# Kernel tuning notes

Measured on AMD Instinct MI355X. Metric: run time of the kernel, lower is better.

The kernel has to match this reference:

```python
import jax, jax.numpy as jnp
import numpy as np

T = 8192          # total prefill tokens (single sequence, cu_seqlens=[0,T])
H = 16            # local num heads (k == v heads)
D = 128           # head_k_dim == head_v_dim
K = 4             # causal conv kernel width
CHUNK = 64        # chunk size used by chunk_kda
EPS = 1e-6


def setup_inputs() -> dict:
    key = jax.random.key(0)
    ks = jax.random.split(key, 6)
    return {
        "mixed_qkv": jax.random.normal(ks[0], (T, 3 * H * D), dtype=jnp.float32),
        "forget_gate": jax.random.normal(ks[1], (T, H * D), dtype=jnp.float32),
        "beta": jax.random.normal(ks[2], (T, H), dtype=jnp.float32),
        "conv_weights": jax.random.normal(ks[3], (3 * H * D, K), dtype=jnp.float32) * 0.1,
        "dt_bias": jax.random.normal(ks[4], (H, D), dtype=jnp.float32),
        "alog": jax.random.normal(ks[5], (H,), dtype=jnp.float32),
    }


def _l2norm(x):
    return x * jax.lax.rsqrt(jnp.sum(x * x, axis=-1, keepdims=True) + EPS)


def _causal_conv1d(x, w):
    # x: [T, C], w: [C, K] depthwise causal conv + SiLU (causal_conv1d_fn)
    xpad = jnp.pad(x, ((K - 1, 0), (0, 0)))
    out = sum(xpad[j:j + T] * w[:, j] for j in range(K))
    return jax.nn.silu(out)


def _kda_forward(mixed_qkv, forget_gate, beta, conv_weights, dt_bias, alog):
    x = _causal_conv1d(mixed_qkv, conv_weights)               # [T, 3*H*D]
    q, k, v = jnp.split(x, [H * D, 2 * H * D], axis=-1)
    q = _l2norm(q.reshape(T, H, D)) * (D ** -0.5)             # scale = head_k_dim^-0.5
    k = _l2norm(k.reshape(T, H, D))
    v = v.reshape(T, H, D)
    # fused_kda_gate: g = -exp(A_log) * softplus(g_raw + dt_bias), per (head, dim)
    g = -jnp.exp(alog)[None, :, None] * jax.nn.softplus(
        forget_gate.reshape(T, H, D) + dt_bias[None])
    decay = jnp.exp(g)                                        # [T, H, D]
    b = jax.nn.sigmoid(beta)                                  # [T, H]

    def step(S, inp):
        # S: [H, Dk, Dv]
        q_t, k_t, v_t, d_t, b_t = inp
        S = S * d_t[:, :, None]                               # per-dim forget gate on key dim
        kmem = jnp.einsum('hk,hkv->hv', k_t, S)
        delta = b_t[:, None] * (v_t - kmem)                   # beta-scaled delta rule
        S = S + jnp.einsum('hk,hv->hkv', k_t, delta)
        o_t = jnp.einsum('hk,hkv->hv', q_t, S)
        return S, o_t

    @jax.checkpoint
    def chunk_fn(S, ch):
        return jax.lax.scan(step, S, ch)

    NC = T // CHUNK
    chunked = lambda a: a.reshape(NC, CHUNK, H, D)
    S0 = jnp.zeros((H, D, D), dtype=jnp.float32)
    _, o = jax.lax.scan(chunk_fn, S0,
                        (chunked(q), chunked(k), chunked(v), chunked(decay),
                         b.reshape(NC, CHUNK, H)))
    return o.reshape(T, H, D)


def reference(mixed_qkv, forget_gate, beta, conv_weights, dt_bias, alog):
    return _kda_forward(mixed_qkv, forget_gate, beta, conv_weights, dt_bias, alog)
```

## Files before the change

### kernel.cpp

```cpp
#include <hip/hip_runtime.h>
#include <math.h>

#define NH 16
#define HD 128
#define CH1 2048
#define CH3 6144
#define CK 64
#define NC 128
#define PCH 132
#define MP 68

#define QT_OFF  0u
#define KBT_OFF 16777216u
#define U0_OFF  33554432u
#define Z_OFF   50331648u
#define W_OFF   67108864u
#define ECG_OFF 75497472u
#define SLAB_OFF 75759616u

__global__ __launch_bounds__(1024, 4)
void kda_chunk(const float* __restrict__ mixed, const float* __restrict__ fg,
               const float* __restrict__ beta, const float* __restrict__ cw,
               const float* __restrict__ dtb, const float* __restrict__ alog,
               float* __restrict__ qt_g, float* __restrict__ kbt_g,
               float* __restrict__ u0_g, float* __restrict__ z_g,
               float* __restrict__ w_g, float* __restrict__ ecg_g) {
  __shared__ float lds[36032];
  float* kL  = lds;
  float* qL  = lds + 8448;
  float* cgL = lds + 16896;
  float* ML  = lds + 25344;
  float* NT  = lds + 29696;
  float* GB  = lds + 34048;
  float* bL  = lds + 34816;
  float* nrm = lds + 34880;

  const int tid = threadIdx.x;
  const int bid = blockIdx.x;
  const int c = bid >> 4, h = bid & 15;
  const int t0 = c * CK;
  const float ea = __expf(alog[h]);

  {
    size_t wb = (size_t)bid * 4096;
#pragma unroll
    for (int i = 0; i < 4; ++i) w_g[wb + tid + 1024 * i] = 0.f;
  }

  for (int it = 0; it < 8; ++it) {
    int cell = tid + (it << 10);
    int d = cell & 127, t = cell >> 7;
    float x = fg[(size_t)(t0 + t) * CH1 + h * HD + d] + dtb[h * HD + d];
    float sp = (x > 20.f) ? x : log1pf(__expf(x));
    cgL[t * PCH + d] = -ea * sp;
  }
  if (tid < 64) bL[tid] = 1.f / (1.f + __expf(-beta[(size_t)(t0 + tid) * NH + h]));
  __syncthreads();

  if (tid < 128) {
    float a = 0.f;
    for (int t = 0; t < 64; ++t) { a += cgL[t * PCH + tid]; cgL[t * PCH + tid] = a; }
    ecg_g[(size_t)bid * 128 + tid] = __expf(a);
  }

  for (int it = 0; it < 16; ++it) {
    int cell = tid + (it << 10);
    int d = cell & 127, sec = (cell >> 7) & 1, t = cell >> 8;
    int ch = sec * CH1 + h * HD + d;
    float4 w4 = ((const float4*)cw)[ch];
    int rbase = t0 + t - 3;
    float acc;
    if (rbase >= 0) {
      const float* mp = mixed + (size_t)rbase * CH3 + ch;
      acc = mp[0] * w4.x + mp[CH3] * w4.y + mp[2 * CH3] * w4.z + mp[3 * CH3] * w4.w;
    } else {
      acc = 0.f;
      if (rbase + 0 >= 0) acc += mixed[(size_t)(rbase + 0) * CH3 + ch] * w4.x;
      if (rbase + 1 >= 0) acc += mixed[(size_t)(rbase + 1) * CH3 + ch] * w4.y;
      if (rbase + 2 >= 0) acc += mixed[(size_t)(rbase + 2) * CH3 + ch] * w4.z;
      acc += mixed[(size_t)(rbase + 3) * CH3 + ch] * w4.w;
    }
    acc = acc / (1.f + __expf(-acc));
    float* dst = (sec == 0) ? qL : kL;
    dst[t * PCH + d] = acc;
  }
  __syncthreads();

  {
    int sec = tid >> 9, t = (tid >> 3) & 63, r = tid & 7;
    const float* src = (sec == 0) ? qL : kL;
    float s = 0.f;
#pragma unroll
    for (int i = 0; i < 4; ++i) {
      float4 v = *(const float4*)(src + t * PCH + r * 16 + i * 4);
      s += v.x * v.x + v.y * v.y + v.z * v.z + v.w * v.w;
    }
    nrm[tid] = s;
  }
  __syncthreads();
  if (tid < 128) {
    int sec = tid >> 6, t = tid & 63;
    float s = 0.f;
#pragma unroll
    for (int r = 0; r < 8; ++r) s += nrm[sec * 512 + t * 8 + r];
    float inv = rsqrtf(s + 1e-6f);
    if (sec == 0) inv *= 0.08838834764831845f;
    nrm[1024 + tid] = inv;
  }
  __syncthreads();
  for (int it = 0; it < 4; ++it) {
    int f4 = tid + (it << 10);
    int sec = f4 >> 11, t = (f4 >> 5) & 63, d4 = f4 & 31;
    float* dst = (sec == 0) ? qL : kL;
    float inv = nrm[1024 + sec * 64 + t];
    float4 v = *(float4*)(dst + t * PCH + d4 * 4);
    v.x *= inv; v.y *= inv; v.z *= inv; v.w *= inv;
    *(float4*)(dst + t * PCH + d4 * 4) = v;
  }
  __syncthreads();

  {
    int tW = tid >> 4, g = tid & 15;
    size_t qb = (size_t)bid * 8192 + (size_t)(g >> 1) * 1024 + tW * 16 + (g & 1) * 8;
    size_t kb = (size_t)bid * 8192;
#pragma unroll
    for (int i = 0; i < 2; ++i) {
      int d = g * 8 + 4 * i;
      float4 qv = *(const float4*)(qL + tW * PCH + d);
      float4 cg4 = *(const float4*)(cgL + tW * PCH + d);
      float4 o;
      o.x = qv.x * __expf(cg4.x); o.y = qv.y * __expf(cg4.y);
      o.z = qv.z * __expf(cg4.z); o.w = qv.w * __expf(cg4.w);
      *(float4*)(qt_g + qb + 4 * i) = o;
      float4 kv = *(const float4*)(kL + tW * PCH + d);
      float4 c63 = *(const float4*)(cgL + 63 * PCH + d);
      kbt_g[kb + (size_t)(d + 0) * 64 + tW] = kv.x * __expf(c63.x - cg4.x);
      kbt_g[kb + (size_t)(d + 1) * 64 + tW] = kv.y * __expf(c63.y - cg4.y);
      kbt_g[kb + (size_t)(d + 2) * 64 + tW] = kv.z * __expf(c63.z - cg4.z);
      kbt_g[kb + (size_t)(d + 3) * 64 + tW] = kv.w * __expf(c63.w - cg4.w);
    }
  }

  if (tid < 544) {
    int L = tid >> 2, dh = tid & 3;
    int tt = (int)((sqrtf(8.f * L + 1.f) - 1.f) * 0.5f);
    while ((tt + 1) * (tt + 2) / 2 <= L) ++tt;
    while (tt * (tt + 1) / 2 > L) --tt;
    int ss = L - tt * (tt + 1) / 2;
    int taD = tt * 4, saD = ss * 4;
    float accA[16], accW[16];
#pragma unroll
    for (int i = 0; i < 16; ++i) { accA[i] = 0.f; accW[i] = 0.f; }
    for (int s4 = 0; s4 < 8; ++s4) {
      int d = (dh << 5) + (((s4 + L + (dh << 1)) & 7) << 2);
      float ks4v[4][4], cs4v[4][4];
#pragma unroll
      for (int j = 0; j < 4; ++j) {
        *(float4*)ks4v[j] = *(const float4*)(kL + (saD + j) * PCH + d);
        *(float4*)cs4v[j] = *(const float4*)(cgL + (saD + j) * PCH + d);
      }
#pragma unroll
      for (int i = 0; i < 4; ++i) {
        float kt4[4], qt4[4], ct4[4];
        *(float4*)kt4 = *(const float4*)(kL + (taD + i) * PCH + d);
        *(float4*)qt4 = *(const float4*)(qL + (taD + i) * PCH + d);
        *(float4*)ct4 = *(const float4*)(cgL + (taD + i) * PCH + d);
#pragma unroll
        for (int j = 0; j < 4; ++j)
#pragma unroll
          for (int dd = 0; dd < 4; ++dd) {
            float diff = ct4[dd] - cs4v[j][dd];
            float e = __expf(fminf(diff, 0.f));
            float m = e * ks4v[j][dd];
            accA[i * 4 + j] += kt4[dd] * m;
            accW[i * 4 + j] += qt4[dd] * m;
          }
      }
    }
#pragma unroll
    for (int i = 0; i < 16; ++i) {
      accA[i] += __shfl_xor(accA[i], 1);
      accA[i] += __shfl_xor(accA[i], 2);
      accW[i] += __shfl_xor(accW[i], 1);
      accW[i] += __shfl_xor(accW[i], 2);
    }
    if (dh == 0) {
      size_t wb = (size_t)bid * 4096;
#pragma unroll
      for (int i = 0; i < 4; ++i)
#pragma unroll
        for (int j = 0; j < 4; ++j) {
          int t = taD + i, s = saD + j;
          if (s < t) ML[t * MP + s] = bL[t] * accA[i * 4 + j];
          float wv = (s <= t) ? accW[i * 4 + j] : 0.f;
          w_g[wb + (size_t)(s >> 3) * 512 + t * 8 + (s & 7)] = wv;
        }
    }
  }
  __syncthreads();

  for (int i = tid; i < 4352; i += 1024) NT[i] = 0.f;
  __syncthreads();
  if (tid < 64) {
    int b4 = tid >> 4, j = tid & 15, bo = b4 * 16;
    NT[(bo + j) * MP + bo + j] = 1.f;
    for (int t = j + 1; t < 16; ++t) {
      float s = 0.f;
      for (int sx = j; sx < t; ++sx)
        s += ML[(bo + t) * MP + bo + sx] * NT[(bo + j) * MP + bo + sx];
      NT[(bo + j) * MP + bo + t] = -s;
    }
  }
  __syncthreads();
  for (int lev = 1; lev <= 3; ++lev) {
    int nb = 4 - lev;
    for (int idx = tid; idx < nb * 256; idx += 1024) {
      int J = idx >> 8, I = J + lev;
      int i = (idx >> 4) & 15, j = idx & 15;
      float s = 0.f;
      for (int P = J; P < I; ++P)
#pragma unroll 4
        for (int p = 0; p < 16; ++p)
          s += ML[(16 * I + i) * MP + 16 * P + p] * NT[(16 * J + j) * MP + 16 * P + p];
      GB[J * 256 + i * 16 + j] = s;
    }
    __syncthreads();
    for (int idx = tid; idx < nb * 256; idx += 1024) {
      int J = idx >> 8, I = J + lev;
      int i = (idx >> 4) & 15, j = idx & 15;
      float s = 0.f;
#pragma unroll 4
      for (int p = 0; p < 16; ++p)
        s += NT[(16 * I + p) * MP + 16 * I + i] * GB[J * 256 + p * 16 + j];
      NT[(16 * J + j) * MP + 16 * I + i] = -s;
    }
    __syncthreads();
  }

  {
    int tW = tid >> 4, g = tid & 15;
    float b = bL[tW];
#pragma unroll
    for (int i = 0; i < 2; ++i) {
      int d = g * 8 + 4 * i;
      float4 kv = *(const float4*)(kL + tW * PCH + d);
      float4 cg4 = *(const float4*)(cgL + tW * PCH + d);
      float4 r;
      r.x = b * kv.x * __expf(cg4.x); r.y = b * kv.y * __expf(cg4.y);
      r.z = b * kv.z * __expf(cg4.z); r.w = b * kv.w * __expf(cg4.w);
      *(float4*)(qL + tW * PCH + d) = r;
    }
  }
  __syncthreads();
  {
    int t2 = tid >> 5, c4 = tid & 31;
    float acc[2][4];
#pragma unroll
    for (int i = 0; i < 2; ++i)
#pragma unroll
      for (int j = 0; j < 4; ++j) acc[i][j] = 0.f;
    for (int s = 0; s < 64; ++s) {
      float2 nv = *(const float2*)(NT + s * MP + t2 * 2);
      float rv[4];
      *(float4*)rv = *(const float4*)(qL + s * PCH + c4 * 4);
#pragma unroll
      for (int j = 0; j < 4; ++j) {
        acc[0][j] += nv.x * rv[j];
        acc[1][j] += nv.y * rv[j];
      }
    }
    size_t zb = (size_t)bid * 8192 + (size_t)(c4 >> 2) * 1024 + (c4 & 3) * 4;
#pragma unroll
    for (int i = 0; i < 2; ++i) {
      float4 o; o.x = acc[i][0]; o.y = acc[i][1]; o.z = acc[i][2]; o.w = acc[i][3];
      *(float4*)(z_g + zb + (size_t)(t2 * 2 + i) * 16) = o;
    }
  }
  __syncthreads();

  for (int it = 0; it < 8; ++it) {
    int cell = tid + (it << 10);
    int d = cell & 127, t = cell >> 7;
    int ch = 2 * CH1 + h * HD + d;
    float4 w4 = ((const float4*)cw)[ch];
    int rbase = t0 + t - 3;
    float acc;
    if (rbase >= 0) {
      const float* mp = mixed + (size_t)rbase * CH3 + ch;
      acc = mp[0] * w4.x + mp[CH3] * w4.y + mp[2 * CH3] * w4.z + mp[3 * CH3] * w4.w;
    } else {
      acc = 0.f;
      if (rbase + 0 >= 0) acc += mixed[(size_t)(rbase + 0) * CH3 + ch] * w4.x;
      if (rbase + 1 >= 0) acc += mixed[(size_t)(rbase + 1) * CH3 + ch] * w4.y;
      if (rbase + 2 >= 0) acc += mixed[(size_t)(rbase + 2) * CH3 + ch] * w4.z;
      acc += mixed[(size_t)(rbase + 3) * CH3 + ch] * w4.w;
    }
    acc = acc / (1.f + __expf(-acc));
    qL[t * PCH + d] = bL[t] * acc;
  }
  __syncthreads();
  {
    int t2 = tid >> 5, c4 = tid & 31;
    float acc[2][4];
#pragma unroll
    for (int i = 0; i < 2; ++i)
#pragma unroll
      for (int j = 0; j < 4; ++j) acc[i][j] = 0.f;
    for (int s = 0; s < 64; ++s) {
      float2 nv = *(const float2*)(NT + s * MP + t2 * 2);
      float rv[4];
      *(float4*)rv = *(const float4*)(qL + s * PCH + c4 * 4);
#pragma unroll
      for (int j = 0; j < 4; ++j) {
        acc[0][j] += nv.x * rv[j];
        acc[1][j] += nv.y * rv[j];
      }
    }
#pragma unroll
    for (int i = 0; i < 2; ++i) {
      size_t ob = ((size_t)(t0 + t2 * 2 + i) * NH + h) * HD + c4 * 4;
      float4 o; o.x = acc[i][0]; o.y = acc[i][1]; o.z = acc[i][2]; o.w = acc[i][3];
      *(float4*)(u0_g + ob) = o;
    }
  }
}

#define PT 68
#define PG 544

__global__ __launch_bounds__(512, 2)
void kda_scan3(const float* __restrict__ qt_g, const float* __restrict__ kbt_g,
               const float* __restrict__ u0_g, const float* __restrict__ z_g,
               const float* __restrict__ w_g, const float* __restrict__ ecg_g,
               float* __restrict__ out, float* __restrict__ slabs) {
  __shared__ float Tp[4352], Op[4352];
  __shared__ float Wp[2176];
  __shared__ float Sl[1536];
  __shared__ float Un[512];
  __shared__ float Ut[544];
  (void)slabs;
  const int tid = threadIdx.x;
  const int bid = blockIdx.x;
  const int h = bid & 15, vg = bid >> 4;
  const int gA = tid >> 6, tA = tid & 63;
  const int tH = (tid & 255) >> 2;
  const int jH = (tid & 3) << 1;
  const int kC = tid & 127;
  const int jq = ((tid >> 7) & 1) << 2;
  const int gB = (tid >> 6) & 3;

  for (int i = tid; i < 1536; i += 512) Sl[i] = 0.f;
  __syncthreads();

  float OsA = 0.f, OsB = 0.f;

  for (int c = 0; c < NC; ++c) {
    const int ch = c * 16 + h;
    float z[16], q[16];
    {
      const float* zb = z_g + (size_t)ch * 8192 + gA * 1024 + tA * 16;
      const float* qb = qt_g + (size_t)ch * 8192 + gA * 1024 + tA * 16;
#pragma unroll
      for (int i = 0; i < 4; ++i) {
        *(float4*)(z + 4 * i) = *(const float4*)(zb + 4 * i);
        *(float4*)(q + 4 * i) = *(const float4*)(qb + 4 * i);
      }
    }
    float w16[16];
    float u0a = 0.f, u0b = 0.f;
    float kv[64], eC = 0.f;
    if (tid < 256) {
      const float* kb = kbt_g + (size_t)ch * 8192 + (size_t)kC * 64;
#pragma unroll
      for (int t4 = 0; t4 < 16; ++t4)
        *(float4*)(kv + 4 * t4) = *(const float4*)(kb + 4 * t4);
      eC = ecg_g[(size_t)ch * 128 + kC];
      const float* ub = u0_g + ((size_t)(c * 64 + tH) * NH + h) * HD + vg * 8 + jH;
      u0a = ub[0]; u0b = ub[1];
    } else {
      const float* wb = w_g + (size_t)ch * 4096 + (size_t)(gB * 2) * 512 + tA * 8;
      *(float4*)w16       = *(const float4*)(wb);
      *(float4*)(w16 + 4) = *(const float4*)(wb + 4);
      *(float4*)(w16 + 8)  = *(const float4*)(wb + 512);
      *(float4*)(w16 + 12) = *(const float4*)(wb + 516);
    }

    if (tid >= 256 && c > 0) {
      float O2a = 0.f, O2b = 0.f;
#pragma unroll
      for (int g = 0; g < 4; ++g) {
        O2a += Wp[g * PG + jH * PT + tH];
        O2b += Wp[g * PG + (jH + 1) * PT + tH];
      }
      float* ob = out + ((size_t)((c - 1) * 64 + tH) * NH + h) * HD + vg * 8 + jH;
      ob[0] = OsA + O2a; ob[1] = OsB + O2b;
    }
    {
      float Ta[8], Oa[8];
#pragma unroll
      for (int j = 0; j < 8; ++j) { Ta[j] = 0.f; Oa[j] = 0.f; }
#pragma unroll
      for (int dd = 0; dd < 16; ++dd) {
        float s8[8];
        const float* sr = Sl + (gA * 16 + dd) * 12;
        *(float4*)s8 = *(const float4*)(sr);
        *(float4*)(s8 + 4) = *(const float4*)(sr + 4);
        float zz = z[dd], qq = q[dd];
#pragma unroll
        for (int j = 0; j < 8; ++j) { Ta[j] += zz * s8[j]; Oa[j] += qq * s8[j]; }
      }
#pragma unroll
      for (int j = 0; j < 8; ++j) {
        Tp[gA * PG + j * PT + tA] = Ta[j];
        Op[gA * PG + j * PT + tA] = Oa[j];
      }
    }
    __syncthreads();

    if (tid < 256) {
      float Tsa = 0.f, Tsb = 0.f;
#pragma unroll
      for (int g = 0; g < 8; ++g) {
        Tsa += Tp[g * PG + jH * PT + tH];
        Tsb += Tp[g * PG + (jH + 1) * PT + tH];
      }
      float Ua = u0a - Tsa, Ub = u0b - Tsb;
      Un[tH * 8 + jH] = Ua; Un[tH * 8 + jH + 1] = Ub;
      Ut[jH * PT + tH] = Ua; Ut[(jH + 1) * PT + tH] = Ub;
    } else {
      float Os1 = 0.f, Os2 = 0.f;
#pragma unroll
      for (int g = 0; g < 8; ++g) {
        Os1 += Op[g * PG + jH * PT + tH];
        Os2 += Op[g * PG + (jH + 1) * PT + tH];
      }
      OsA = Os1; OsB = Os2;
    }
    __syncthreads();

    if (tid < 256) {
      float a0 = 0.f, a1 = 0.f, a2 = 0.f, a3 = 0.f;
      const float* u0r = Ut + (jq + 0) * PT;
      const float* u1r = Ut + (jq + 1) * PT;
      const float* u2r = Ut + (jq + 2) * PT;
      const float* u3r = Ut + (jq + 3) * PT;
#pragma unroll
      for (int t4 = 0; t4 < 16; ++t4) {
        float k0 = kv[4 * t4], k1 = kv[4 * t4 + 1], k2 = kv[4 * t4 + 2], k3 = kv[4 * t4 + 3];
        float4 ua = *(const float4*)(u0r + 4 * t4);
        float4 ub = *(const float4*)(u1r + 4 * t4);
        float4 uc = *(const float4*)(u2r + 4 * t4);
        float4 ud = *(const float4*)(u3r + 4 * t4);
        a0 += k0 * ua.x + k1 * ua.y + k2 * ua.z + k3 * ua.w;
        a1 += k0 * ub.x + k1 * ub.y + k2 * ub.z + k3 * ub.w;
        a2 += k0 * uc.x + k1 * uc.y + k2 * uc.z + k3 * uc.w;
        a3 += k0 * ud.x + k1 * ud.y + k2 * ud.z + k3 * ud.w;
      }
      float* sp = Sl + kC * 12 + jq;
      float4 s = *(float4*)sp;
      s.x = eC * s.x + a0; s.y = eC * s.y + a1;
      s.z = eC * s.z + a2; s.w = eC * s.w + a3;
      *(float4*)sp = s;
    } else {
      float Wa[8];
#pragma unroll
      for (int j = 0; j < 8; ++j) Wa[j] = 0.f;
#pragma unroll
      for (int sp = 0; sp < 16; ++sp) {
        const float* ur = Un + (gB * 16 + sp) * 8;
        float u8[8];
        *(float4*)u8 = *(const float4*)(ur);
        *(float4*)(u8 + 4) = *(const float4*)(ur + 4);
        float wv = w16[sp];
#pragma unroll
        for (int j = 0; j < 8; ++j) Wa[j] += wv * u8[j];
      }
#pragma unroll
      for (int j = 0; j < 8; ++j) Wp[gB * PG + j * PT + tA] = Wa[j];
    }
    __syncthreads();
  }

  if (tid >= 256) {
    float O2a = 0.f, O2b = 0.f;
#pragma unroll
    for (int g = 0; g < 4; ++g) {
      O2a += Wp[g * PG + jH * PT + tH];
      O2b += Wp[g * PG + (jH + 1) * PT + tH];
    }
    float* ob = out + ((size_t)((NC - 1) * 64 + tH) * NH + h) * HD + vg * 8 + jH;
    ob[0] = OsA + O2a; ob[1] = OsB + O2b;
  }
}

extern "C" void kernel_launch(void* const* d_in, const int* in_sizes, int n_in,
                              void* d_out, int out_size, void* d_ws, size_t ws_size,
                              hipStream_t stream) {
  const float* mixed = (const float*)d_in[0];
  const float* fg    = (const float*)d_in[1];
  const float* beta  = (const float*)d_in[2];
  const float* cw    = (const float*)d_in[3];
  const float* dtb   = (const float*)d_in[4];
  const float* alog  = (const float*)d_in[5];
  float* ws = (float*)d_ws;
  float* qt_g  = ws + QT_OFF;
  float* kbt_g = ws + KBT_OFF;
  float* u0_g  = ws + U0_OFF;
  float* z_g   = ws + Z_OFF;
  float* w_g   = ws + W_OFF;
  float* ecg_g = ws + ECG_OFF;
  float* slabs = ws + SLAB_OFF;

  hipLaunchKernelGGL(kda_chunk, dim3(NC * NH), dim3(1024), 0, stream,
                     mixed, fg, beta, cw, dtb, alog,
                     qt_g, kbt_g, u0_g, z_g, w_g, ecg_g);
  hipLaunchKernelGGL(kda_scan3, dim3(256), dim3(512), 0, stream,
                     qt_g, kbt_g, u0_g, z_g, w_g, ecg_g, (float*)d_out, slabs);
  (void)in_sizes; (void)n_in; (void)out_size; (void)ws_size;
}
```

Before: 1.621 ms.

## Double scan kernel threads to 1024, halving per-thread work in sequential chunk loop

The sequential per-chunk scan kernel now runs with 1024 threads per block instead of 512. Each thread handles half as many reduction terms, state columns and output elements, and the shared partial-sum buffers double to hold the extra partials. The goal is to shorten the latency-bound serial chain over 128 chunks by spreading each step across more wavefronts. In exchange, barriers cost more, shared memory grows and the reduction fan-in is larger.

```diff
diff --git a/kernel.cpp b/kernel.cpp
--- a/kernel.cpp
+++ b/kernel.cpp
@@ -328,13 +328,13 @@
 #define PT 68
 #define PG 544
 
-__global__ __launch_bounds__(512, 2)
+__global__ __launch_bounds__(1024, 4)
 void kda_scan3(const float* __restrict__ qt_g, const float* __restrict__ kbt_g,
                const float* __restrict__ u0_g, const float* __restrict__ z_g,
                const float* __restrict__ w_g, const float* __restrict__ ecg_g,
                float* __restrict__ out, float* __restrict__ slabs) {
-  __shared__ float Tp[4352], Op[4352];
-  __shared__ float Wp[2176];
+  __shared__ float Tp[8704], Op[8704];
+  __shared__ float Wp[4352];
   __shared__ float Sl[1536];
   __shared__ float Un[512];
   __shared__ float Ut[544];
@@ -343,69 +343,59 @@
   const int bid = blockIdx.x;
   const int h = bid & 15, vg = bid >> 4;
   const int gA = tid >> 6, tA = tid & 63;
-  const int tH = (tid & 255) >> 2;
-  const int jH = (tid & 3) << 1;
+  const int tH = (tid >> 3) & 63, jS = tid & 7;
   const int kC = tid & 127;
-  const int jq = ((tid >> 7) & 1) << 2;
-  const int gB = (tid >> 6) & 3;
-
-  for (int i = tid; i < 1536; i += 512) Sl[i] = 0.f;
-  __syncthreads();
-
-  float OsA = 0.f, OsB = 0.f;
+  const int jp = (tid >> 7) & 3;
+  const int gB = (tid >> 6) & 7;
+
+  for (int i = tid; i < 1536; i += 1024) Sl[i] = 0.f;
+  __syncthreads();
+
+  float OsV = 0.f;
 
   for (int c = 0; c < NC; ++c) {
     const int ch = c * 16 + h;
-    float z[16], q[16];
+    float z8[8], q8[8];
     {
-      const float* zb = z_g + (size_t)ch * 8192 + gA * 1024 + tA * 16;
-      const float* qb = qt_g + (size_t)ch * 8192 + gA * 1024 + tA * 16;
-#pragma unroll
-      for (int i = 0; i < 4; ++i) {
-        *(float4*)(z + 4 * i) = *(const float4*)(zb + 4 * i);
-        *(float4*)(q + 4 * i) = *(const float4*)(qb + 4 * i);
-      }
-    }
-    float w16[16];
-    float u0a = 0.f, u0b = 0.f;
-    float kv[64], eC = 0.f;
-    if (tid < 256) {
+      const size_t base = (size_t)ch * 8192 + (size_t)(gA >> 1) * 1024 + tA * 16 + (gA & 1) * 8;
+      const float* zb = z_g + base;
+      const float* qb = qt_g + base;
+      *(float4*)z8       = *(const float4*)(zb);
+      *(float4*)(z8 + 4) = *(const float4*)(zb + 4);
+      *(float4*)q8       = *(const float4*)(qb);
+      *(float4*)(q8 + 4) = *(const float4*)(qb + 4);
+    }
+    float kv[64], eC = 0.f, u0v = 0.f, w8[8];
+    if (tid < 512) {
       const float* kb = kbt_g + (size_t)ch * 8192 + (size_t)kC * 64;
 #pragma unroll
       for (int t4 = 0; t4 < 16; ++t4)
         *(float4*)(kv + 4 * t4) = *(const float4*)(kb + 4 * t4);
       eC = ecg_g[(size_t)ch * 128 + kC];
-      const float* ub = u0_g + ((size_t)(c * 64 + tH) * NH + h) * HD + vg * 8 + jH;
-      u0a = ub[0]; u0b = ub[1];
+      u0v = u0_g[((size_t)(c * 64 + tH) * NH + h) * HD + vg * 8 + jS];
     } else {
-      const float* wb = w_g + (size_t)ch * 4096 + (size_t)(gB * 2) * 512 + tA * 8;
-      *(float4*)w16       = *(const float4*)(wb);
-      *(float4*)(w16 + 4) = *(const float4*)(wb + 4);
-      *(float4*)(w16 + 8)  = *(const float4*)(wb + 512);
-      *(float4*)(w16 + 12) = *(const float4*)(wb + 516);
-    }
-
-    if (tid >= 256 && c > 0) {
-      float O2a = 0.f, O2b = 0.f;
-#pragma unroll
-      for (int g = 0; g < 4; ++g) {
-        O2a += Wp[g * PG + jH * PT + tH];
-        O2b += Wp[g * PG + (jH + 1) * PT + tH];
-      }
-      float* ob = out + ((size_t)((c - 1) * 64 + tH) * NH + h) * HD + vg * 8 + jH;
-      ob[0] = OsA + O2a; ob[1] = OsB + O2b;
+      const float* wb = w_g + (size_t)ch * 4096 + (size_t)gB * 512 + tA * 8;
+      *(float4*)w8       = *(const float4*)(wb);
+      *(float4*)(w8 + 4) = *(const float4*)(wb + 4);
+    }
+
+    if (tid >= 512 && c > 0) {
+      float O2 = 0.f;
+#pragma unroll
+      for (int g = 0; g < 8; ++g) O2 += Wp[g * PG + jS * PT + tH];
+      out[((size_t)((c - 1) * 64 + tH) * NH + h) * HD + vg * 8 + jS] = OsV + O2;
     }
     {
       float Ta[8], Oa[8];
 #pragma unroll
       for (int j = 0; j < 8; ++j) { Ta[j] = 0.f; Oa[j] = 0.f; }
 #pragma unroll
-      for (int dd = 0; dd < 16; ++dd) {
+      for (int dd = 0; dd < 8; ++dd) {
         float s8[8];
-        const float* sr = Sl + (gA * 16 + dd) * 12;
+        const float* sr = Sl + (gA * 8 + dd) * 12;
         *(float4*)s8 = *(const float4*)(sr);
         *(float4*)(s8 + 4) = *(const float4*)(sr + 4);
-        float zz = z[dd], qq = q[dd];
+        float zz = z8[dd], qq = q8[dd];
 #pragma unroll
         for (int j = 0; j < 8; ++j) { Ta[j] += zz * s8[j]; Oa[j] += qq * s8[j]; }
       }
@@ -417,61 +407,49 @@
     }
     __syncthreads();
 
-    if (tid < 256) {
-      float Tsa = 0.f, Tsb = 0.f;
-#pragma unroll
-      for (int g = 0; g < 8; ++g) {
-        Tsa += Tp[g * PG + jH * PT + tH];
-        Tsb += Tp[g * PG + (jH + 1) * PT + tH];
-      }
-      float Ua = u0a - Tsa, Ub = u0b - Tsb;
-      Un[tH * 8 + jH] = Ua; Un[tH * 8 + jH + 1] = Ub;
-      Ut[jH * PT + tH] = Ua; Ut[(jH + 1) * PT + tH] = Ub;
+    if (tid < 512) {
+      float Ts = 0.f;
+#pragma unroll
+      for (int g = 0; g < 16; ++g) Ts += Tp[g * PG + jS * PT + tH];
+      float U = u0v - Ts;
+      Un[tH * 8 + jS] = U;
+      Ut[jS * PT + tH] = U;
     } else {
-      float Os1 = 0.f, Os2 = 0.f;
-#pragma unroll
-      for (int g = 0; g < 8; ++g) {
-        Os1 += Op[g * PG + jH * PT + tH];
-        Os2 += Op[g * PG + (jH + 1) * PT + tH];
-      }
-      OsA = Os1; OsB = Os2;
+      float Os = 0.f;
+#pragma unroll
+      for (int g = 0; g < 16; ++g) Os += Op[g * PG + jS * PT + tH];
+      OsV = Os;
     }
     __syncthreads();
 
-    if (tid < 256) {
-      float a0 = 0.f, a1 = 0.f, a2 = 0.f, a3 = 0.f;
-      const float* u0r = Ut + (jq + 0) * PT;
-      const float* u1r = Ut + (jq + 1) * PT;
-      const float* u2r = Ut + (jq + 2) * PT;
-      const float* u3r = Ut + (jq + 3) * PT;
+    if (tid < 512) {
+      float a0 = 0.f, a1 = 0.f;
+      const float* u0r = Ut + (2 * jp) * PT;
+      const float* u1r = Ut + (2 * jp + 1) * PT;
 #pragma unroll
       for (int t4 = 0; t4 < 16; ++t4) {
         float k0 = kv[4 * t4], k1 = kv[4 * t4 + 1], k2 = kv[4 * t4 + 2], k3 = kv[4 * t4 + 3];
         float4 ua = *(const float4*)(u0r + 4 * t4);
         float4 ub = *(const float4*)(u1r + 4 * t4);
-        float4 uc = *(const float4*)(u2r + 4 * t4);
-        float4 ud = *(const float4*)(u3r + 4 * t4);
         a0 += k0 * ua.x + k1 * ua.y + k2 * ua.z + k3 * ua.w;
         a1 += k0 * ub.x + k1 * ub.y + k2 * ub.z + k3 * ub.w;
-        a2 += k0 * uc.x + k1 * uc.y + k2 * uc.z + k3 * uc.w;
-        a3 += k0 * ud.x + k1 * ud.y + k2 * ud.z + k3 * ud.w;
-      }
-      float* sp = Sl + kC * 12 + jq;
-      float4 s = *(float4*)sp;
-      s.x = eC * s.x + a0; s.y = eC * s.y + a1;
-      s.z = eC * s.z + a2; s.w = eC * s.w + a3;
-      *(float4*)sp = s;
+      }
+      float* sp = Sl + kC * 12 + 2 * jp;
+      float2 s = *(float2*)sp;
+      s.x = eC * s.x + a0;
+      s.y = eC * s.y + a1;
+      *(float2*)sp = s;
     } else {
       float Wa[8];
 #pragma unroll
       for (int j = 0; j < 8; ++j) Wa[j] = 0.f;
 #pragma unroll
-      for (int sp = 0; sp < 16; ++sp) {
-        const float* ur = Un + (gB * 16 + sp) * 8;
+      for (int sp = 0; sp < 8; ++sp) {
+        const float* ur = Un + (gB * 8 + sp) * 8;
         float u8[8];
         *(float4*)u8 = *(const float4*)(ur);
         *(float4*)(u8 + 4) = *(const float4*)(ur + 4);
-        float wv = w16[sp];
+        float wv = w8[sp];
 #pragma unroll
         for (int j = 0; j < 8; ++j) Wa[j] += wv * u8[j];
       }
@@ -481,15 +459,11 @@
     __syncthreads();
   }
 
-  if (tid >= 256) {
-    float O2a = 0.f, O2b = 0.f;
-#pragma unroll
-    for (int g = 0; g < 4; ++g) {
-      O2a += Wp[g * PG + jH * PT + tH];
-      O2b += Wp[g * PG + (jH + 1) * PT + tH];
-    }
-    float* ob = out + ((size_t)((NC - 1) * 64 + tH) * NH + h) * HD + vg * 8 + jH;
-    ob[0] = OsA + O2a; ob[1] = OsB + O2b;
+  if (tid >= 512) {
+    float O2 = 0.f;
+#pragma unroll
+    for (int g = 0; g < 8; ++g) O2 += Wp[g * PG + jS * PT + tH];
+    out[((size_t)((NC - 1) * 64 + tH) * NH + h) * HD + vg * 8 + jS] = OsV + O2;
   }
 }
 
@@ -514,7 +488,7 @@
   hipLaunchKernelGGL(kda_chunk, dim3(NC * NH), dim3(1024), 0, stream,
                      mixed, fg, beta, cw, dtb, alog,
                      qt_g, kbt_g, u0_g, z_g, w_g, ecg_g);
-  hipLaunchKernelGGL(kda_scan3, dim3(256), dim3(512), 0, stream,
+  hipLaunchKernelGGL(kda_scan3, dim3(256), dim3(1024), 0, stream,
                      qt_g, kbt_g, u0_g, z_g, w_g, ecg_g, (float*)d_out, slabs);
   (void)in_sizes; (void)n_in; (void)out_size; (void)ws_size;
 }
```

Measured after the change: 2.002 ms. +23.5%, slower.
